# Optimization experiments

Hardware: AMD Instinct MI355X
Metric: run time of the kernel (lower is better)

Reference implementation:

```python
import jax, jax.numpy as jnp
import numpy as np

B, CIN, T, H, W = 2, 256, 16, 16, 8
FF, COUT, NHEADS = 512, 256, 8
TEMP = 16.0
BN_EPS = 1e-5


def setup_inputs() -> dict:
    key = jax.random.key(0)
    ks = jax.random.split(key, 6)
    s_in = 1.0 / np.sqrt(CIN)
    s_ff = 1.0 / np.sqrt(FF)
    return {
        "x": jax.random.normal(ks[0], (B, CIN, T, H, W), jnp.float32),
        "WK": jax.random.uniform(ks[1], (FF, CIN), jnp.float32, -s_in, s_in),
        "WQ": jax.random.uniform(ks[2], (FF, CIN), jnp.float32, -s_in, s_in),
        "WV": jax.random.uniform(ks[3], (FF, CIN), jnp.float32, -s_in, s_in),
        "Wo": jax.random.uniform(ks[4], (COUT, FF), jnp.float32, -s_ff, s_ff),
        "bo": jax.random.uniform(ks[5], (COUT,), jnp.float32, -s_ff, s_ff),
        "gamma": jnp.ones((COUT,), jnp.float32),
        "beta": jnp.zeros((COUT,), jnp.float32),
    }


def reference(x, WK, WQ, WV, Wo, bo, gamma, beta):
    N = T * H * W
    xf = x.reshape(B, CIN, N)  # 1x1 conv3d == channel matmul
    dh = FF // NHEADS
    K = jnp.einsum("fc,bcn->bfn", WK, xf).reshape(B, NHEADS, dh, N)
    Q = jnp.einsum("fc,bcn->bfn", WQ, xf).reshape(B, NHEADS, dh, N)
    V = jnp.einsum("fc,bcn->bfn", WV, xf).reshape(B, NHEADS, dh, N)
    # KQ[b,h,i,j] = K_i . Q_j  (i = key token, j = query token, as in torch)
    KQ = jnp.einsum("bhdi,bhdj->bhij", K, Q) / TEMP
    # block-causal mask: token time index t = token_idx // (H*W); tril -> allow i >= j
    t_idx = jnp.arange(N) // (H * W)
    allow = t_idx[:, None] >= t_idx[None, :]  # (N, N)
    KQ = jnp.where(allow[None, None], KQ, -jnp.inf)
    attn = jax.nn.softmax(KQ, axis=3)  # softmax over j (last dim), as in torch
    # out[b,h,d,i] = sum_j V[b,h,d,j] * attn[b,h,i,j]
    Vo = jnp.einsum("bhdj,bhij->bhdi", V, attn).reshape(B, FF, N)
    y = jnp.einsum("of,bfn->bon", Wo, Vo) + bo[None, :, None]
    y = jax.nn.relu(y).reshape(B, COUT, T, H, W)
    out = x + y  # skip: out_dim == in_dim
    # BatchNorm3d (training-mode batch stats, biased var)
    mean = out.mean(axis=(0, 2, 3, 4), keepdims=True)
    var = out.var(axis=(0, 2, 3, 4), keepdims=True)
    norm = (out - mean) * jax.lax.rsqrt(var + BN_EPS)
    return norm * gamma[None, :, None, None, None] + beta[None, :, None, None, None]
```

## Files before the change

### kernel.cpp

```cpp
#include <hip/hip_runtime.h>
#include <math.h>

#define BB_   2
#define CIN_  256
#define NTOK_ 2048
#define FF_   512
#define COUT_ 256
#define NH_   8
#define DH_   64
#define HW_   128
#define BNEPS_ 1e-5f
#define SCALE_LOG2_ 0.09016844005556021f

typedef __attribute__((ext_vector_type(8))) short short8;
typedef __attribute__((ext_vector_type(4))) short bfx4;
typedef __attribute__((ext_vector_type(4))) float f32x4;

#if __has_builtin(__builtin_amdgcn_mfma_f32_16x16x16_bf16)
#define MFMA16(a, b, c) __builtin_amdgcn_mfma_f32_16x16x16_bf16(a, b, c, 0, 0, 0)
#else
#define MFMA16(a, b, c) __builtin_amdgcn_mfma_f32_16x16x16bf16_1k(a, b, c, 0, 0, 0)
#endif

__device__ inline unsigned short f2bf(float f) {
  union { float f; unsigned u; } v; v.f = f;
  unsigned r = (v.u + 0x7FFF + ((v.u >> 16) & 1)) >> 16;
  return (unsigned short)r;
}

__device__ __forceinline__ void dma16(const unsigned short* g, unsigned short* l) {
  __builtin_amdgcn_global_load_lds(
      (const __attribute__((address_space(1))) void*)g,
      (__attribute__((address_space(3))) void*)l, 16, 0, 0);
}

__global__ __launch_bounds__(256) void prep_kernel(
    const float* __restrict__ x, const float* __restrict__ WK,
    const float* __restrict__ WQ, const float* __restrict__ WV,
    const float* __restrict__ Wo, unsigned short* __restrict__ xT,
    unsigned short* __restrict__ Wkb, unsigned short* __restrict__ Wqb,
    unsigned short* __restrict__ Wvb, unsigned short* __restrict__ Wob) {
  __shared__ float T[64 * 65];
  const int tid = threadIdx.x;
  const int bid = blockIdx.x;
  if (bid < 256) {
    const int b = bid >> 7;
    const int rem = bid & 127;
    const int n0 = (rem >> 2) * 64;
    const int c0 = (rem & 3) * 64;
#pragma unroll
    for (int p = 0; p < 4; ++p) {
      const int idx = tid + 256 * p;
      const int row = idx >> 4, col = (idx & 15) * 4;
      const float4 v =
          *(const float4*)(x + (size_t)(b * CIN_ + c0 + row) * NTOK_ + n0 + col);
      T[row * 65 + col + 0] = v.x; T[row * 65 + col + 1] = v.y;
      T[row * 65 + col + 2] = v.z; T[row * 65 + col + 3] = v.w;
    }
    __syncthreads();
#pragma unroll
    for (int p = 0; p < 2; ++p) {
      const int idx = tid + 256 * p;
      const int nl = idx >> 3, c8 = (idx & 7) * 8;
      unsigned short u[8];
#pragma unroll
      for (int i = 0; i < 8; ++i) u[i] = f2bf(T[(c8 + i) * 65 + nl]);
      *(uint4*)(xT + ((size_t)(b * NTOK_ + n0 + nl)) * CIN_ + c0 + c8) =
          *(uint4*)u;
    }
  } else {
    const int t = bid - 256;
    const int which = t >> 5, blk = t & 31;
    const float* src = which == 0 ? WK : which == 1 ? WQ : which == 2 ? WV : Wo;
    unsigned short* dst = which == 0 ? Wkb : which == 1 ? Wqb : which == 2 ? Wvb : Wob;
    const int base = blk * 4096 + tid * 16;
#pragma unroll
    for (int p = 0; p < 4; ++p) {
      const float4 v = *(const float4*)(src + base + p * 4);
      ushort4 u;
      u.x = f2bf(v.x); u.y = f2bf(v.y); u.z = f2bf(v.z); u.w = f2bf(v.w);
      *(ushort4*)(dst + base + p * 4) = u;
    }
  }
}

__global__ __launch_bounds__(256, 3) void qkv_kernel(
    const unsigned short* __restrict__ xT, const unsigned short* __restrict__ Wkb,
    const unsigned short* __restrict__ Wqb, const unsigned short* __restrict__ Wvb,
    unsigned short* __restrict__ Kb, unsigned short* __restrict__ Qb,
    unsigned short* __restrict__ Vt) {
  __shared__ unsigned short Wsh[128 * 72];
  __shared__ unsigned short Xsh[64 * 72];
  const int tid = threadIdx.x;
  const int lane = tid & 63, w = tid >> 6;
  const int lx = lane & 15, q = lane >> 4;
  const int wm = w >> 1, wn = w & 1;
  const int n0 = blockIdx.x * 64;
  const int f0 = blockIdx.y * 128;
  const int b = blockIdx.z / 3, which = blockIdx.z % 3;
  const unsigned short* Wb = which == 0 ? Wkb : which == 1 ? Wqb : Wvb;

  const int srow = tid >> 3;
  const int soff = (tid & 7) * 8;
  const unsigned short* Wg = Wb + (size_t)(f0 + srow) * CIN_ + soff;
  const unsigned short* Xg = xT + ((size_t)(b * NTOK_ + n0 + srow)) * CIN_ + soff;

  uint4 wr[4], xr[2];
#pragma unroll
  for (int r = 0; r < 4; ++r) wr[r] = *(const uint4*)(Wg + (size_t)(32 * r) * CIN_);
#pragma unroll
  for (int r = 0; r < 2; ++r) xr[r] = *(const uint4*)(Xg + (size_t)(32 * r) * CIN_);

  f32x4 acc[4][2];
#pragma unroll
  for (int i = 0; i < 4; ++i)
#pragma unroll
    for (int j = 0; j < 2; ++j) acc[i][j] = (f32x4){0.f, 0.f, 0.f, 0.f};

  for (int kk = 0; kk < 4; ++kk) {
    __syncthreads();
#pragma unroll
    for (int r = 0; r < 4; ++r) *(uint4*)(Wsh + (srow + 32 * r) * 72 + soff) = wr[r];
#pragma unroll
    for (int r = 0; r < 2; ++r) *(uint4*)(Xsh + (srow + 32 * r) * 72 + soff) = xr[r];
    if (kk < 3) {
      const int c0 = (kk + 1) * 64;
#pragma unroll
      for (int r = 0; r < 4; ++r) wr[r] = *(const uint4*)(Wg + (size_t)(32 * r) * CIN_ + c0);
#pragma unroll
      for (int r = 0; r < 2; ++r) xr[r] = *(const uint4*)(Xg + (size_t)(32 * r) * CIN_ + c0);
    }
    __syncthreads();
    short8 xF[2][2];
#pragma unroll
    for (int i = 0; i < 2; ++i) {
      xF[i][0] = *(const short8*)(Xsh + (32 * wn + 16 * i + lx) * 72 + q * 8);
      xF[i][1] = *(const short8*)(Xsh + (32 * wn + 16 * i + lx) * 72 + 32 + q * 8);
    }
    if (which < 2) {
#pragma unroll
      for (int i = 0; i < 4; ++i) {
        const short8 w0 = *(const short8*)(Wsh + (64 * wm + 16 * i + lx) * 72 + q * 8);
        const short8 w1 = *(const short8*)(Wsh + (64 * wm + 16 * i + lx) * 72 + 32 + q * 8);
#pragma unroll
        for (int j = 0; j < 2; ++j) {
          acc[i][j] = __builtin_amdgcn_mfma_f32_16x16x32_bf16(w0, xF[j][0], acc[i][j], 0, 0, 0);
          acc[i][j] = __builtin_amdgcn_mfma_f32_16x16x32_bf16(w1, xF[j][1], acc[i][j], 0, 0, 0);
        }
      }
    } else {
#pragma unroll
      for (int jf = 0; jf < 4; ++jf) {
        const short8 w0 = *(const short8*)(Wsh + (64 * wm + 16 * jf + lx) * 72 + q * 8);
        const short8 w1 = *(const short8*)(Wsh + (64 * wm + 16 * jf + lx) * 72 + 32 + q * 8);
#pragma unroll
        for (int i = 0; i < 2; ++i) {
          acc[jf][i] = __builtin_amdgcn_mfma_f32_16x16x32_bf16(xF[i][0], w0, acc[jf][i], 0, 0, 0);
          acc[jf][i] = __builtin_amdgcn_mfma_f32_16x16x32_bf16(xF[i][1], w1, acc[jf][i], 0, 0, 0);
        }
      }
    }
  }

  const int h = (f0 >> 6) + wm;
  if (which < 2) {
    unsigned short* Y = (which == 0 ? Kb : Qb);
    const float sc = (which == 0) ? SCALE_LOG2_ : 1.0f;
#pragma unroll
    for (int i = 0; i < 4; ++i)
#pragma unroll
      for (int j = 0; j < 2; ++j) {
        const int n = n0 + 32 * wn + 16 * j + lx;
        const int d0 = 16 * i + 4 * q;
        ushort4 u;
        u.x = f2bf(acc[i][j][0] * sc); u.y = f2bf(acc[i][j][1] * sc);
        u.z = f2bf(acc[i][j][2] * sc); u.w = f2bf(acc[i][j][3] * sc);
        *(ushort4*)(Y + ((size_t)((b * NH_ + h) * NTOK_ + n)) * DH_ + d0) = u;
      }
  } else {
#pragma unroll
    for (int jf = 0; jf < 4; ++jf)
#pragma unroll
      for (int i = 0; i < 2; ++i) {
        const int d = 16 * jf + lx;
        const int n = n0 + 32 * wn + 16 * i + 4 * q;
        ushort4 u;
        u.x = f2bf(acc[jf][i][0]); u.y = f2bf(acc[jf][i][1]);
        u.z = f2bf(acc[jf][i][2]); u.w = f2bf(acc[jf][i][3]);
        *(ushort4*)(Vt + ((size_t)((b * NH_ + h) * DH_ + d)) * NTOK_ + n) = u;
      }
  }
}

__global__ __launch_bounds__(256, 2) void attn_kernel(
    const unsigned short* __restrict__ Kb, const unsigned short* __restrict__ Qb,
    const unsigned short* __restrict__ Vt, unsigned short* __restrict__ Ob) {
  __shared__ __align__(16) unsigned short Qbuf[2][8192];
  __shared__ __align__(16) unsigned short Vbuf[2][8192];

  const int tid = threadIdx.x;
  const int lane = tid & 63;
  const int w = tid >> 6;
  const int lx = lane & 15;
  const int g = lane >> 4;

  const int bid = blockIdx.x;
  const int u = bid >> 4;
  const int iblk = (u < 16) ? (31 - u) : (u - 16);
  const int bh = bid & 15;
  const int h = bh & 7, b = bh >> 3;
  const int i0 = iblk * 64;
  const int njt = (iblk >> 1) + 1;

  const size_t bhs = (size_t)b * NH_ + h;
  const unsigned short* Kg = Kb + bhs * (size_t)NTOK_ * DH_ + (size_t)i0 * DH_;
  const unsigned short* Qg = Qb + bhs * (size_t)NTOK_ * DH_;
  const unsigned short* Vg = Vt + bhs * (size_t)DH_ * NTOK_;

  auto stage = [&](int buf, int j0) {
#pragma unroll
    for (int cc = 0; cc < 4; ++cc) {
      const int chunk = 4 * w + cc;
      {
        const int row = chunk * 8 + (lane >> 3);
        const int grp = (lane & 7) ^ (row & 7);
        dma16(Qg + (size_t)(j0 + row) * DH_ + grp * 8, &Qbuf[buf][chunk * 512]);
      }
      {
        const int row = chunk * 4 + (lane >> 4);
        const int grp = (lane & 15) ^ (row & 7);
        dma16(Vg + (size_t)row * NTOK_ + j0 + grp * 8, &Vbuf[buf][chunk * 512]);
      }
    }
  };

  const short8 aK0 = *(const short8*)(Kg + (16 * w + lx) * DH_ + g * 8);
  const short8 aK1 = *(const short8*)(Kg + (16 * w + lx) * DH_ + 32 + g * 8);

  f32x4 o[4];
#pragma unroll
  for (int t = 0; t < 4; ++t) o[t] = (f32x4){0.f, 0.f, 0.f, 0.f};
  float rs = 0.f;

  const int fr0 = ((g ^ (lx & 7)) << 3);
  const int fr1 = (((4 + g) ^ (lx & 7)) << 3);

  stage(0, 0);
  __syncthreads();

  int cur = 0;
  for (int jt = 0; jt < njt; ++jt) {
    if (jt + 1 < njt) stage(cur ^ 1, (jt + 1) * 128);

    const unsigned short* Qs = Qbuf[cur];
    const unsigned short* Vs = Vbuf[cur];

    f32x4 sa[8];
#pragma unroll
    for (int s = 0; s < 8; ++s) {
      const int row = 16 * s + lx;
      const short8 a0 = *(const short8*)(Qs + row * 64 + fr0);
      const short8 a1 = *(const short8*)(Qs + row * 64 + fr1);
      sa[s] = (f32x4){0.f, 0.f, 0.f, 0.f};
      sa[s] = __builtin_amdgcn_mfma_f32_16x16x32_bf16(a0, aK0, sa[s], 0, 0, 0);
      sa[s] = __builtin_amdgcn_mfma_f32_16x16x32_bf16(a1, aK1, sa[s], 0, 0, 0);
    }

#pragma unroll
    for (int s = 0; s < 8; ++s) {
      const float p0 = __builtin_amdgcn_exp2f(sa[s][0]);
      const float p1 = __builtin_amdgcn_exp2f(sa[s][1]);
      const float p2 = __builtin_amdgcn_exp2f(sa[s][2]);
      const float p3 = __builtin_amdgcn_exp2f(sa[s][3]);
      rs += (p0 + p1) + (p2 + p3);
      union { unsigned u[2]; bfx4 v; } pk;
      pk.u[0] = (__builtin_bit_cast(unsigned, p0) >> 16) |
                (__builtin_bit_cast(unsigned, p1) & 0xFFFF0000u);
      pk.u[1] = (__builtin_bit_cast(unsigned, p2) >> 16) |
                (__builtin_bit_cast(unsigned, p3) & 0xFFFF0000u);
      const int jgrp = 2 * s + (g >> 1);
      const int joff = (g & 1) << 2;
#pragma unroll
      for (int t = 0; t < 4; ++t) {
        const int row = 16 * t + lx;
        const bfx4 va = *(const bfx4*)(Vs + row * 128 +
                                       ((jgrp ^ (row & 7)) << 3) + joff);
        o[t] = MFMA16(va, pk.v, o[t]);
      }
    }

    __syncthreads();
    cur ^= 1;
  }

  rs += __shfl_xor(rs, 16);
  rs += __shfl_xor(rs, 32);
  const float invl = 1.0f / rs;
  const int n = i0 + 16 * w + lx;
#pragma unroll
  for (int t = 0; t < 4; ++t) {
    ushort4 uo;
    uo.x = f2bf(o[t][0] * invl); uo.y = f2bf(o[t][1] * invl);
    uo.z = f2bf(o[t][2] * invl); uo.w = f2bf(o[t][3] * invl);
    *(ushort4*)(Ob + ((size_t)(b * NTOK_ + n)) * FF_ + h * 64 + 16 * t + 4 * g) = uo;
  }
}

__global__ __launch_bounds__(256) void proj_kernel(
    const unsigned short* __restrict__ Ob, const unsigned short* __restrict__ Wob,
    const float* __restrict__ bo, const float* __restrict__ x,
    float* __restrict__ pre) {
  __shared__ unsigned short Osh[64 * 72];
  __shared__ unsigned short Wsh[64 * 72];
  const int tid = threadIdx.x;
  const int lane = tid & 63, w = tid >> 6;
  const int lx = lane & 15, q = lane >> 4;
  const int wn = w & 1, wo = w >> 1;
  const int n0 = blockIdx.x * 64;
  const int o0 = blockIdx.y * 64;
  const int b = blockIdx.z;

  const int srow = tid >> 3;
  const int soff = (tid & 7) * 8;
  const unsigned short* Og = Ob + ((size_t)(b * NTOK_ + n0 + srow)) * FF_ + soff;
  const unsigned short* Wg = Wob + (size_t)(o0 + srow) * FF_ + soff;

  uint4 orr[2], wrr[2];
#pragma unroll
  for (int r = 0; r < 2; ++r) {
    orr[r] = *(const uint4*)(Og + (size_t)(32 * r) * FF_);
    wrr[r] = *(const uint4*)(Wg + (size_t)(32 * r) * FF_);
  }

  f32x4 acc[2][2];
#pragma unroll
  for (int i = 0; i < 2; ++i)
#pragma unroll
    for (int j = 0; j < 2; ++j) acc[i][j] = (f32x4){0.f, 0.f, 0.f, 0.f};

  for (int kk = 0; kk < 8; ++kk) {
    __syncthreads();
#pragma unroll
    for (int r = 0; r < 2; ++r) {
      *(uint4*)(Osh + (srow + 32 * r) * 72 + soff) = orr[r];
      *(uint4*)(Wsh + (srow + 32 * r) * 72 + soff) = wrr[r];
    }
    if (kk < 7) {
      const int c0 = (kk + 1) * 64;
#pragma unroll
      for (int r = 0; r < 2; ++r) {
        orr[r] = *(const uint4*)(Og + (size_t)(32 * r) * FF_ + c0);
        wrr[r] = *(const uint4*)(Wg + (size_t)(32 * r) * FF_ + c0);
      }
    }
    __syncthreads();
    short8 aF[2][2], bF[2][2];
#pragma unroll
    for (int i = 0; i < 2; ++i) {
      aF[i][0] = *(const short8*)(Osh + (32 * wn + 16 * i + lx) * 72 + q * 8);
      aF[i][1] = *(const short8*)(Osh + (32 * wn + 16 * i + lx) * 72 + 32 + q * 8);
      bF[i][0] = *(const short8*)(Wsh + (32 * wo + 16 * i + lx) * 72 + q * 8);
      bF[i][1] = *(const short8*)(Wsh + (32 * wo + 16 * i + lx) * 72 + 32 + q * 8);
    }
#pragma unroll
    for (int i = 0; i < 2; ++i)
#pragma unroll
      for (int j = 0; j < 2; ++j) {
        acc[i][j] = __builtin_amdgcn_mfma_f32_16x16x32_bf16(aF[i][0], bF[j][0], acc[i][j], 0, 0, 0);
        acc[i][j] = __builtin_amdgcn_mfma_f32_16x16x32_bf16(aF[i][1], bF[j][1], acc[i][j], 0, 0, 0);
      }
  }

#pragma unroll
  for (int j = 0; j < 2; ++j) {
    const int o = o0 + 32 * wo + 16 * j + lx;
    const float bias = bo[o];
#pragma unroll
    for (int i = 0; i < 2; ++i) {
      const int n = n0 + 32 * wn + 16 * i + 4 * q;
      const float4 xv = *(const float4*)(x + ((size_t)(b * CIN_ + o)) * NTOK_ + n);
      float4 v;
      v.x = fmaxf(acc[i][j][0] + bias, 0.f) + xv.x;
      v.y = fmaxf(acc[i][j][1] + bias, 0.f) + xv.y;
      v.z = fmaxf(acc[i][j][2] + bias, 0.f) + xv.z;
      v.w = fmaxf(acc[i][j][3] + bias, 0.f) + xv.w;
      *(float4*)(pre + ((size_t)(b * COUT_ + o)) * NTOK_ + n) = v;
    }
  }
}

__global__ __launch_bounds__(256) void bn_kernel(
    float* __restrict__ out, const float* __restrict__ gamma,
    const float* __restrict__ beta) {
  __shared__ float red[8];
  const int c = blockIdx.x;
  const int tid = threadIdx.x;
  const int lane = tid & 63, w = tid >> 6;

  float4 v[2][2];
  float s = 0.f, s2 = 0.f;
#pragma unroll
  for (int b = 0; b < BB_; ++b) {
    float* base = out + ((size_t)(b * COUT_ + c)) * NTOK_;
#pragma unroll
    for (int p = 0; p < 2; ++p) {
      const float4 t = *(const float4*)(base + 4 * tid + p * 1024);
      v[b][p] = t;
      s += t.x + t.y + t.z + t.w;
      s2 += t.x * t.x + t.y * t.y + t.z * t.z + t.w * t.w;
    }
  }
#pragma unroll
  for (int off = 32; off >= 1; off >>= 1) {
    s += __shfl_xor(s, off);
    s2 += __shfl_xor(s2, off);
  }
  if (lane == 0) { red[w] = s; red[4 + w] = s2; }
  __syncthreads();
  const float S = red[0] + red[1] + red[2] + red[3];
  const float S2 = red[4] + red[5] + red[6] + red[7];
  const float inv = 1.0f / (float)(BB_ * NTOK_);
  const float mean = S * inv;
  const float var = S2 * inv - mean * mean;
  const float sc = rsqrtf(var + BNEPS_) * gamma[c];
  const float bt = beta[c];
#pragma unroll
  for (int b = 0; b < BB_; ++b) {
    float* base = out + ((size_t)(b * COUT_ + c)) * NTOK_;
#pragma unroll
    for (int p = 0; p < 2; ++p) {
      float4 t = v[b][p];
      t.x = (t.x - mean) * sc + bt;
      t.y = (t.y - mean) * sc + bt;
      t.z = (t.z - mean) * sc + bt;
      t.w = (t.w - mean) * sc + bt;
      *(float4*)(base + 4 * tid + p * 1024) = t;
    }
  }
}

extern "C" void kernel_launch(void* const* d_in, const int* in_sizes, int n_in,
                              void* d_out, int out_size, void* d_ws, size_t ws_size,
                              hipStream_t stream) {
  (void)in_sizes; (void)n_in; (void)out_size; (void)ws_size;
  const float* x = (const float*)d_in[0];
  const float* WK = (const float*)d_in[1];
  const float* WQ = (const float*)d_in[2];
  const float* WV = (const float*)d_in[3];
  const float* Wo = (const float*)d_in[4];
  const float* bo = (const float*)d_in[5];
  const float* gamma = (const float*)d_in[6];
  const float* beta = (const float*)d_in[7];

  char* ws = (char*)d_ws;
  unsigned short* xT  = (unsigned short*)(ws);
  unsigned short* Wkb = (unsigned short*)(ws + 2097152);
  unsigned short* Wqb = (unsigned short*)(ws + 2359296);
  unsigned short* Wvb = (unsigned short*)(ws + 2621440);
  unsigned short* Wob = (unsigned short*)(ws + 2883584);
  unsigned short* Kb  = (unsigned short*)(ws + 3145728);
  unsigned short* Qb  = (unsigned short*)(ws + 7340032);
  unsigned short* Vt  = (unsigned short*)(ws + 11534336);
  unsigned short* Ob  = (unsigned short*)(ws + 15728640);
  float* out = (float*)d_out;

  prep_kernel<<<384, 256, 0, stream>>>(x, WK, WQ, WV, Wo, xT, Wkb, Wqb, Wvb, Wob);
  qkv_kernel<<<dim3(32, 4, 6), 256, 0, stream>>>(xT, Wkb, Wqb, Wvb, Kb, Qb, Vt);
  attn_kernel<<<dim3(512, 1, 1), 256, 0, stream>>>(Kb, Qb, Vt, Ob);
  proj_kernel<<<dim3(32, 4, 2), 256, 0, stream>>>(Ob, Wob, bo, x, out);
  bn_kernel<<<256, 256, 0, stream>>>(out, gamma, beta);
}
```

Before: 139.9 us.

## Split attention key-tile columns across waves and reduce partial outputs in LDS

```diff
diff --git a/kernel.cpp b/kernel.cpp
--- a/kernel.cpp
+++ b/kernel.cpp
@@ -21,6 +21,7 @@
 #else
 #define MFMA16(a, b, c) __builtin_amdgcn_mfma_f32_16x16x16bf16_1k(a, b, c, 0, 0, 0)
 #endif
+#define MFMA32(a, b, c) __builtin_amdgcn_mfma_f32_16x16x32_bf16(a, b, c, 0, 0, 0)
 
 __device__ inline unsigned short f2bf(float f) {
   union { float f; unsigned u; } v; v.f = f;
@@ -144,8 +145,8 @@
         const short8 w1 = *(const short8*)(Wsh + (64 * wm + 16 * i + lx) * 72 + 32 + q * 8);
 #pragma unroll
         for (int j = 0; j < 2; ++j) {
-          acc[i][j] = __builtin_amdgcn_mfma_f32_16x16x32_bf16(w0, xF[j][0], acc[i][j], 0, 0, 0);
-          acc[i][j] = __builtin_amdgcn_mfma_f32_16x16x32_bf16(w1, xF[j][1], acc[i][j], 0, 0, 0);
+          acc[i][j] = MFMA32(w0, xF[j][0], acc[i][j]);
+          acc[i][j] = MFMA32(w1, xF[j][1], acc[i][j]);
         }
       }
     } else {
@@ -155,8 +156,8 @@
         const short8 w1 = *(const short8*)(Wsh + (64 * wm + 16 * jf + lx) * 72 + 32 + q * 8);
 #pragma unroll
         for (int i = 0; i < 2; ++i) {
-          acc[jf][i] = __builtin_amdgcn_mfma_f32_16x16x32_bf16(xF[i][0], w0, acc[jf][i], 0, 0, 0);
-          acc[jf][i] = __builtin_amdgcn_mfma_f32_16x16x32_bf16(xF[i][1], w1, acc[jf][i], 0, 0, 0);
+          acc[jf][i] = MFMA32(xF[i][0], w0, acc[jf][i]);
+          acc[jf][i] = MFMA32(xF[i][1], w1, acc[jf][i]);
         }
       }
     }
@@ -195,8 +196,7 @@
 __global__ __launch_bounds__(256, 2) void attn_kernel(
     const unsigned short* __restrict__ Kb, const unsigned short* __restrict__ Qb,
     const unsigned short* __restrict__ Vt, unsigned short* __restrict__ Ob) {
-  __shared__ __align__(16) unsigned short Qbuf[2][8192];
-  __shared__ __align__(16) unsigned short Vbuf[2][8192];
+  __shared__ __align__(16) char smem[70656];
 
   const int tid = threadIdx.x;
   const int lane = tid & 63;
@@ -224,23 +224,31 @@
       {
         const int row = chunk * 8 + (lane >> 3);
         const int grp = (lane & 7) ^ (row & 7);
-        dma16(Qg + (size_t)(j0 + row) * DH_ + grp * 8, &Qbuf[buf][chunk * 512]);
+        dma16(Qg + (size_t)(j0 + row) * DH_ + grp * 8,
+              (unsigned short*)(smem + buf * 16384) + chunk * 512);
       }
       {
         const int row = chunk * 4 + (lane >> 4);
         const int grp = (lane & 15) ^ (row & 7);
-        dma16(Vg + (size_t)row * NTOK_ + j0 + grp * 8, &Vbuf[buf][chunk * 512]);
+        dma16(Vg + (size_t)row * NTOK_ + j0 + grp * 8,
+              (unsigned short*)(smem + 32768 + buf * 16384) + chunk * 512);
       }
     }
   };
 
-  const short8 aK0 = *(const short8*)(Kg + (16 * w + lx) * DH_ + g * 8);
-  const short8 aK1 = *(const short8*)(Kg + (16 * w + lx) * DH_ + 32 + g * 8);
-
-  f32x4 o[4];
-#pragma unroll
-  for (int t = 0; t < 4; ++t) o[t] = (f32x4){0.f, 0.f, 0.f, 0.f};
-  float rs = 0.f;
+  short8 aK[4][2];
+#pragma unroll
+  for (int ic = 0; ic < 4; ++ic) {
+    aK[ic][0] = *(const short8*)(Kg + (16 * ic + lx) * DH_ + g * 8);
+    aK[ic][1] = *(const short8*)(Kg + (16 * ic + lx) * DH_ + 32 + g * 8);
+  }
+
+  f32x4 o[4][4];
+#pragma unroll
+  for (int t = 0; t < 4; ++t)
+#pragma unroll
+    for (int ic = 0; ic < 4; ++ic) o[t][ic] = (f32x4){0.f, 0.f, 0.f, 0.f};
+  float rs[4] = {0.f, 0.f, 0.f, 0.f};
 
   const int fr0 = ((g ^ (lx & 7)) << 3);
   const int fr1 = (((4 + g) ^ (lx & 7)) << 3);
@@ -252,40 +260,45 @@
   for (int jt = 0; jt < njt; ++jt) {
     if (jt + 1 < njt) stage(cur ^ 1, (jt + 1) * 128);
 
-    const unsigned short* Qs = Qbuf[cur];
-    const unsigned short* Vs = Vbuf[cur];
-
-    f32x4 sa[8];
-#pragma unroll
-    for (int s = 0; s < 8; ++s) {
-      const int row = 16 * s + lx;
-      const short8 a0 = *(const short8*)(Qs + row * 64 + fr0);
-      const short8 a1 = *(const short8*)(Qs + row * 64 + fr1);
-      sa[s] = (f32x4){0.f, 0.f, 0.f, 0.f};
-      sa[s] = __builtin_amdgcn_mfma_f32_16x16x32_bf16(a0, aK0, sa[s], 0, 0, 0);
-      sa[s] = __builtin_amdgcn_mfma_f32_16x16x32_bf16(a1, aK1, sa[s], 0, 0, 0);
-    }
-
-#pragma unroll
-    for (int s = 0; s < 8; ++s) {
-      const float p0 = __builtin_amdgcn_exp2f(sa[s][0]);
-      const float p1 = __builtin_amdgcn_exp2f(sa[s][1]);
-      const float p2 = __builtin_amdgcn_exp2f(sa[s][2]);
-      const float p3 = __builtin_amdgcn_exp2f(sa[s][3]);
-      rs += (p0 + p1) + (p2 + p3);
-      union { unsigned u[2]; bfx4 v; } pk;
-      pk.u[0] = (__builtin_bit_cast(unsigned, p0) >> 16) |
-                (__builtin_bit_cast(unsigned, p1) & 0xFFFF0000u);
-      pk.u[1] = (__builtin_bit_cast(unsigned, p2) >> 16) |
-                (__builtin_bit_cast(unsigned, p3) & 0xFFFF0000u);
-      const int jgrp = 2 * s + (g >> 1);
+    const unsigned short* Qs = (const unsigned short*)(smem + cur * 16384);
+    const unsigned short* Vs = (const unsigned short*)(smem + 32768 + cur * 16384);
+
+#pragma unroll
+    for (int jc = 0; jc < 2; ++jc) {
+      const int jrow = 32 * w + 16 * jc + lx;
+      const short8 a0 = *(const short8*)(Qs + jrow * 64 + fr0);
+      const short8 a1 = *(const short8*)(Qs + jrow * 64 + fr1);
+      f32x4 sa[4];
+#pragma unroll
+      for (int ic = 0; ic < 4; ++ic) {
+        sa[ic] = (f32x4){0.f, 0.f, 0.f, 0.f};
+        sa[ic] = MFMA32(a0, aK[ic][0], sa[ic]);
+        sa[ic] = MFMA32(a1, aK[ic][1], sa[ic]);
+      }
+      bfx4 pk[4];
+#pragma unroll
+      for (int ic = 0; ic < 4; ++ic) {
+        const float p0 = __builtin_amdgcn_exp2f(sa[ic][0]);
+        const float p1 = __builtin_amdgcn_exp2f(sa[ic][1]);
+        const float p2 = __builtin_amdgcn_exp2f(sa[ic][2]);
+        const float p3 = __builtin_amdgcn_exp2f(sa[ic][3]);
+        rs[ic] += (p0 + p1) + (p2 + p3);
+        union { unsigned u[2]; bfx4 v; } pkk;
+        pkk.u[0] = (__builtin_bit_cast(unsigned, p0) >> 16) |
+                   (__builtin_bit_cast(unsigned, p1) & 0xFFFF0000u);
+        pkk.u[1] = (__builtin_bit_cast(unsigned, p2) >> 16) |
+                   (__builtin_bit_cast(unsigned, p3) & 0xFFFF0000u);
+        pk[ic] = pkk.v;
+      }
+      const int jgrp = 4 * w + 2 * jc + (g >> 1);
       const int joff = (g & 1) << 2;
 #pragma unroll
       for (int t = 0; t < 4; ++t) {
-        const int row = 16 * t + lx;
-        const bfx4 va = *(const bfx4*)(Vs + row * 128 +
-                                       ((jgrp ^ (row & 7)) << 3) + joff);
-        o[t] = MFMA16(va, pk.v, o[t]);
+        const int vrow = 16 * t + lx;
+        const bfx4 va = *(const bfx4*)(Vs + vrow * 128 +
+                                       ((jgrp ^ (vrow & 7)) << 3) + joff);
+#pragma unroll
+        for (int ic = 0; ic < 4; ++ic) o[t][ic] = MFMA16(va, pk[ic], o[t][ic]);
       }
     }
 
@@ -293,17 +306,45 @@
     cur ^= 1;
   }
 
-  rs += __shfl_xor(rs, 16);
-  rs += __shfl_xor(rs, 32);
-  const float invl = 1.0f / rs;
-  const int n = i0 + 16 * w + lx;
-#pragma unroll
-  for (int t = 0; t < 4; ++t) {
-    ushort4 uo;
-    uo.x = f2bf(o[t][0] * invl); uo.y = f2bf(o[t][1] * invl);
-    uo.z = f2bf(o[t][2] * invl); uo.w = f2bf(o[t][3] * invl);
-    *(ushort4*)(Ob + ((size_t)(b * NTOK_ + n)) * FF_ + h * 64 + 16 * t + 4 * g) = uo;
-  }
+  float* Ored = (float*)smem;
+  float* Lsum = (float*)(smem + 69632);
+#pragma unroll
+  for (int t = 0; t < 4; ++t)
+#pragma unroll
+    for (int ic = 0; ic < 4; ++ic)
+      *(f32x4*)(Ored + w * 4352 + (16 * ic + lx) * 68 + 16 * t + 4 * g) = o[t][ic];
+#pragma unroll
+  for (int ic = 0; ic < 4; ++ic) {
+    rs[ic] += __shfl_xor(rs[ic], 16);
+    rs[ic] += __shfl_xor(rs[ic], 32);
+  }
+  if (lane < 16) {
+#pragma unroll
+    for (int ic = 0; ic < 4; ++ic) Lsum[w * 64 + 16 * ic + lx] = rs[ic];
+  }
+  __syncthreads();
+
+  const int i = tid >> 2;
+  const int dq = (tid & 3) * 16;
+  const float l = Lsum[i] + Lsum[64 + i] + Lsum[128 + i] + Lsum[192 + i];
+  const float invl = 1.0f / l;
+  union { unsigned short us[16]; uint4 q[2]; } ob;
+#pragma unroll
+  for (int k = 0; k < 4; ++k) {
+    const f32x4 v0 = *(const f32x4*)(Ored + 0 * 4352 + i * 68 + dq + 4 * k);
+    const f32x4 v1 = *(const f32x4*)(Ored + 1 * 4352 + i * 68 + dq + 4 * k);
+    const f32x4 v2 = *(const f32x4*)(Ored + 2 * 4352 + i * 68 + dq + 4 * k);
+    const f32x4 v3 = *(const f32x4*)(Ored + 3 * 4352 + i * 68 + dq + 4 * k);
+    const f32x4 s4 = (v0 + v1) + (v2 + v3);
+    ob.us[4 * k + 0] = f2bf(s4[0] * invl);
+    ob.us[4 * k + 1] = f2bf(s4[1] * invl);
+    ob.us[4 * k + 2] = f2bf(s4[2] * invl);
+    ob.us[4 * k + 3] = f2bf(s4[3] * invl);
+  }
+  const int n = i0 + i;
+  unsigned short* dst = Ob + ((size_t)(b * NTOK_ + n)) * FF_ + h * 64 + dq;
+  *(uint4*)(dst) = ob.q[0];
+  *(uint4*)(dst + 8) = ob.q[1];
 }
 
 __global__ __launch_bounds__(256) void proj_kernel(
@@ -366,8 +407,8 @@
     for (int i = 0; i < 2; ++i)
 #pragma unroll
       for (int j = 0; j < 2; ++j) {
-        acc[i][j] = __builtin_amdgcn_mfma_f32_16x16x32_bf16(aF[i][0], bF[j][0], acc[i][j], 0, 0, 0);
-        acc[i][j] = __builtin_amdgcn_mfma_f32_16x16x32_bf16(aF[i][1], bF[j][1], acc[i][j], 0, 0, 0);
+        acc[i][j] = MFMA32(aF[i][0], bF[j][0], acc[i][j]);
+        acc[i][j] = MFMA32(aF[i][1], bF[j][1], acc[i][j]);
       }
   }
 
```

After: 141.9 us. Within noise of the previous version (+1.4%).

## Pair long and short causal query tiles per attention block

Applied to the files above, without the earlier changes.

```diff
diff --git a/kernel.cpp b/kernel.cpp
--- a/kernel.cpp
+++ b/kernel.cpp
@@ -21,6 +21,7 @@
 #else
 #define MFMA16(a, b, c) __builtin_amdgcn_mfma_f32_16x16x16bf16_1k(a, b, c, 0, 0, 0)
 #endif
+#define MFMA32(a, b, c) __builtin_amdgcn_mfma_f32_16x16x32_bf16(a, b, c, 0, 0, 0)
 
 __device__ inline unsigned short f2bf(float f) {
   union { float f; unsigned u; } v; v.f = f;
@@ -144,8 +145,8 @@
         const short8 w1 = *(const short8*)(Wsh + (64 * wm + 16 * i + lx) * 72 + 32 + q * 8);
 #pragma unroll
         for (int j = 0; j < 2; ++j) {
-          acc[i][j] = __builtin_amdgcn_mfma_f32_16x16x32_bf16(w0, xF[j][0], acc[i][j], 0, 0, 0);
-          acc[i][j] = __builtin_amdgcn_mfma_f32_16x16x32_bf16(w1, xF[j][1], acc[i][j], 0, 0, 0);
+          acc[i][j] = MFMA32(w0, xF[j][0], acc[i][j]);
+          acc[i][j] = MFMA32(w1, xF[j][1], acc[i][j]);
         }
       }
     } else {
@@ -155,8 +156,8 @@
         const short8 w1 = *(const short8*)(Wsh + (64 * wm + 16 * jf + lx) * 72 + 32 + q * 8);
 #pragma unroll
         for (int i = 0; i < 2; ++i) {
-          acc[jf][i] = __builtin_amdgcn_mfma_f32_16x16x32_bf16(xF[i][0], w0, acc[jf][i], 0, 0, 0);
-          acc[jf][i] = __builtin_amdgcn_mfma_f32_16x16x32_bf16(xF[i][1], w1, acc[jf][i], 0, 0, 0);
+          acc[jf][i] = MFMA32(xF[i][0], w0, acc[jf][i]);
+          acc[jf][i] = MFMA32(xF[i][1], w1, acc[jf][i]);
         }
       }
     }
@@ -204,16 +205,13 @@
   const int lx = lane & 15;
   const int g = lane >> 4;
 
-  const int bid = blockIdx.x;
-  const int u = bid >> 4;
-  const int iblk = (u < 16) ? (31 - u) : (u - 16);
-  const int bh = bid & 15;
+  const int k = blockIdx.x;
+  const int t = k >> 4;
+  const int bh = k & 15;
   const int h = bh & 7, b = bh >> 3;
-  const int i0 = iblk * 64;
-  const int njt = (iblk >> 1) + 1;
 
   const size_t bhs = (size_t)b * NH_ + h;
-  const unsigned short* Kg = Kb + bhs * (size_t)NTOK_ * DH_ + (size_t)i0 * DH_;
+  const unsigned short* Kbase = Kb + bhs * (size_t)NTOK_ * DH_;
   const unsigned short* Qg = Qb + bhs * (size_t)NTOK_ * DH_;
   const unsigned short* Vg = Vt + bhs * (size_t)DH_ * NTOK_;
 
@@ -234,75 +232,84 @@
     }
   };
 
-  const short8 aK0 = *(const short8*)(Kg + (16 * w + lx) * DH_ + g * 8);
-  const short8 aK1 = *(const short8*)(Kg + (16 * w + lx) * DH_ + 32 + g * 8);
-
-  f32x4 o[4];
-#pragma unroll
-  for (int t = 0; t < 4; ++t) o[t] = (f32x4){0.f, 0.f, 0.f, 0.f};
-  float rs = 0.f;
-
   const int fr0 = ((g ^ (lx & 7)) << 3);
   const int fr1 = (((4 + g) ^ (lx & 7)) << 3);
 
-  stage(0, 0);
-  __syncthreads();
-
-  int cur = 0;
-  for (int jt = 0; jt < njt; ++jt) {
-    if (jt + 1 < njt) stage(cur ^ 1, (jt + 1) * 128);
-
-    const unsigned short* Qs = Qbuf[cur];
-    const unsigned short* Vs = Vbuf[cur];
-
-    f32x4 sa[8];
-#pragma unroll
-    for (int s = 0; s < 8; ++s) {
-      const int row = 16 * s + lx;
-      const short8 a0 = *(const short8*)(Qs + row * 64 + fr0);
-      const short8 a1 = *(const short8*)(Qs + row * 64 + fr1);
-      sa[s] = (f32x4){0.f, 0.f, 0.f, 0.f};
-      sa[s] = __builtin_amdgcn_mfma_f32_16x16x32_bf16(a0, aK0, sa[s], 0, 0, 0);
-      sa[s] = __builtin_amdgcn_mfma_f32_16x16x32_bf16(a1, aK1, sa[s], 0, 0, 0);
-    }
-
-#pragma unroll
-    for (int s = 0; s < 8; ++s) {
-      const float p0 = __builtin_amdgcn_exp2f(sa[s][0]);
-      const float p1 = __builtin_amdgcn_exp2f(sa[s][1]);
-      const float p2 = __builtin_amdgcn_exp2f(sa[s][2]);
-      const float p3 = __builtin_amdgcn_exp2f(sa[s][3]);
-      rs += (p0 + p1) + (p2 + p3);
-      union { unsigned u[2]; bfx4 v; } pk;
-      pk.u[0] = (__builtin_bit_cast(unsigned, p0) >> 16) |
-                (__builtin_bit_cast(unsigned, p1) & 0xFFFF0000u);
-      pk.u[1] = (__builtin_bit_cast(unsigned, p2) >> 16) |
-                (__builtin_bit_cast(unsigned, p3) & 0xFFFF0000u);
-      const int jgrp = 2 * s + (g >> 1);
-      const int joff = (g & 1) << 2;
-#pragma unroll
-      for (int t = 0; t < 4; ++t) {
-        const int row = 16 * t + lx;
-        const bfx4 va = *(const bfx4*)(Vs + row * 128 +
-                                       ((jgrp ^ (row & 7)) << 3) + joff);
-        o[t] = MFMA16(va, pk.v, o[t]);
-      }
-    }
-
-    __syncthreads();
-    cur ^= 1;
-  }
-
-  rs += __shfl_xor(rs, 16);
-  rs += __shfl_xor(rs, 32);
-  const float invl = 1.0f / rs;
-  const int n = i0 + 16 * w + lx;
-#pragma unroll
-  for (int t = 0; t < 4; ++t) {
-    ushort4 uo;
-    uo.x = f2bf(o[t][0] * invl); uo.y = f2bf(o[t][1] * invl);
-    uo.z = f2bf(o[t][2] * invl); uo.w = f2bf(o[t][3] * invl);
-    *(ushort4*)(Ob + ((size_t)(b * NTOK_ + n)) * FF_ + h * 64 + 16 * t + 4 * g) = uo;
+#pragma unroll 1
+  for (int ph = 0; ph < 2; ++ph) {
+    const int iblk = ph ? t : 31 - t;
+    const int i0 = iblk * 64;
+    const int njt = (iblk >> 1) + 1;
+
+    const unsigned short* Kg = Kbase + (size_t)i0 * DH_;
+    const short8 aK0 = *(const short8*)(Kg + (16 * w + lx) * DH_ + g * 8);
+    const short8 aK1 = *(const short8*)(Kg + (16 * w + lx) * DH_ + 32 + g * 8);
+
+    f32x4 o[4];
+#pragma unroll
+    for (int tt = 0; tt < 4; ++tt) o[tt] = (f32x4){0.f, 0.f, 0.f, 0.f};
+    float rs = 0.f;
+
+    stage(0, 0);
+    __syncthreads();
+
+    int cur = 0;
+    for (int jt = 0; jt < njt; ++jt) {
+      if (jt + 1 < njt) stage(cur ^ 1, (jt + 1) * 128);
+
+      const unsigned short* Qs = Qbuf[cur];
+      const unsigned short* Vs = Vbuf[cur];
+
+      f32x4 sa[8];
+#pragma unroll
+      for (int s = 0; s < 8; ++s) {
+        const int row = 16 * s + lx;
+        const short8 a0 = *(const short8*)(Qs + row * 64 + fr0);
+        const short8 a1 = *(const short8*)(Qs + row * 64 + fr1);
+        sa[s] = (f32x4){0.f, 0.f, 0.f, 0.f};
+        sa[s] = MFMA32(a0, aK0, sa[s]);
+        sa[s] = MFMA32(a1, aK1, sa[s]);
+      }
+
+#pragma unroll
+      for (int s = 0; s < 8; ++s) {
+        const float p0 = __builtin_amdgcn_exp2f(sa[s][0]);
+        const float p1 = __builtin_amdgcn_exp2f(sa[s][1]);
+        const float p2 = __builtin_amdgcn_exp2f(sa[s][2]);
+        const float p3 = __builtin_amdgcn_exp2f(sa[s][3]);
+        rs += (p0 + p1) + (p2 + p3);
+        union { unsigned u[2]; bfx4 v; } pk;
+        pk.u[0] = (__builtin_bit_cast(unsigned, p0) >> 16) |
+                  (__builtin_bit_cast(unsigned, p1) & 0xFFFF0000u);
+        pk.u[1] = (__builtin_bit_cast(unsigned, p2) >> 16) |
+                  (__builtin_bit_cast(unsigned, p3) & 0xFFFF0000u);
+        const int jgrp = 2 * s + (g >> 1);
+        const int joff = (g & 1) << 2;
+#pragma unroll
+        for (int tt = 0; tt < 4; ++tt) {
+          const int row = 16 * tt + lx;
+          const bfx4 va = *(const bfx4*)(Vbuf[cur] + row * 128 +
+                                         ((jgrp ^ (row & 7)) << 3) + joff);
+          o[tt] = MFMA16(va, pk.v, o[tt]);
+        }
+      }
+      (void)Vs;
+
+      __syncthreads();
+      cur ^= 1;
+    }
+
+    rs += __shfl_xor(rs, 16);
+    rs += __shfl_xor(rs, 32);
+    const float invl = 1.0f / rs;
+    const int n = i0 + 16 * w + lx;
+#pragma unroll
+    for (int tt = 0; tt < 4; ++tt) {
+      ushort4 uo;
+      uo.x = f2bf(o[tt][0] * invl); uo.y = f2bf(o[tt][1] * invl);
+      uo.z = f2bf(o[tt][2] * invl); uo.w = f2bf(o[tt][3] * invl);
+      *(ushort4*)(Ob + ((size_t)(b * NTOK_ + n)) * FF_ + h * 64 + 16 * tt + 4 * g) = uo;
+    }
   }
 }
 
@@ -366,8 +373,8 @@
     for (int i = 0; i < 2; ++i)
 #pragma unroll
       for (int j = 0; j < 2; ++j) {
-        acc[i][j] = __builtin_amdgcn_mfma_f32_16x16x32_bf16(aF[i][0], bF[j][0], acc[i][j], 0, 0, 0);
-        acc[i][j] = __builtin_amdgcn_mfma_f32_16x16x32_bf16(aF[i][1], bF[j][1], acc[i][j], 0, 0, 0);
+        acc[i][j] = MFMA32(aF[i][0], bF[j][0], acc[i][j]);
+        acc[i][j] = MFMA32(aF[i][1], bF[j][1], acc[i][j]);
       }
   }
 
@@ -466,7 +473,7 @@
 
   prep_kernel<<<384, 256, 0, stream>>>(x, WK, WQ, WV, Wo, xT, Wkb, Wqb, Wvb, Wob);
   qkv_kernel<<<dim3(32, 4, 6), 256, 0, stream>>>(xT, Wkb, Wqb, Wvb, Kb, Qb, Vt);
-  attn_kernel<<<dim3(512, 1, 1), 256, 0, stream>>>(Kb, Qb, Vt, Ob);
+  attn_kernel<<<dim3(256, 1, 1), 256, 0, stream>>>(Kb, Qb, Vt, Ob);
   proj_kernel<<<dim3(32, 4, 2), 256, 0, stream>>>(Ob, Wob, bo, x, out);
   bn_kernel<<<256, 256, 0, stream>>>(out, gamma, beta);
 }
```

New measurement: 143.2 us. 2.4% more time.
